# Optimization experiments

Hardware: AMD Instinct MI355X
Metric: run time of the kernel (lower is better)

The kernel has to match this reference:

```python
import jax, jax.numpy as jnp
import numpy as np

B = 256
H, W = 8, 16          # input_resolution for channels=256
C = 768               # dim = channels*3
WS = 4                # window_size
SHIFT = 2             # shift_size
NH = 12               # num_heads
HD = C // NH          # head_dim = 64
HID = 1024            # mlp hidden = channels*4
N = WS * WS           # tokens per window = 16
NW = (H // WS) * (W // WS)  # windows per image = 8
LN_EPS = 1e-5


def _rel_pos_index():
    coords = np.stack(np.meshgrid(np.arange(WS), np.arange(WS), indexing='ij'))  # [2,ws,ws]
    cf = coords.reshape(2, -1)                      # [2, N]
    rel = (cf[:, :, None] - cf[:, None, :]).transpose(1, 2, 0)  # [N, N, 2]
    rel[:, :, 0] += WS - 1
    rel[:, :, 1] += WS - 1
    rel[:, :, 0] *= 2 * WS - 1
    return jnp.asarray(rel.sum(-1))                 # [N, N] int


def _attn_mask():
    img = np.zeros((H, W))
    slices = (slice(0, -WS), slice(-WS, -SHIFT), slice(-SHIFT, None))
    cnt = 0
    for hs in slices:
        for ws_ in slices:
            img[hs, ws_] = cnt
            cnt += 1
    mw = img.reshape(H // WS, WS, W // WS, WS).transpose(0, 2, 1, 3).reshape(-1, N)  # [nW, N]
    am = mw[:, None, :] - mw[:, :, None]            # [nW, N, N]
    return jnp.asarray(np.where(am != 0, -100.0, 0.0).astype(np.float32))


REL_IDX = _rel_pos_index()
ATTN_MASK = _attn_mask()


def _ln(x, g, b):
    m = x.mean(-1, keepdims=True)
    v = ((x - m) ** 2).mean(-1, keepdims=True)
    return (x - m) / jnp.sqrt(v + LN_EPS) * g + b


def setup_inputs() -> dict:
    key = jax.random.key(0)
    ks = jax.random.split(key, 8)
    s = 0.02
    return {
        'x': jax.random.normal(ks[0], (B, H * W, C), jnp.float32),
        'ln1_g': jnp.ones((C,), jnp.float32),
        'ln1_b': jnp.zeros((C,), jnp.float32),
        'qkv_w': jax.random.normal(ks[1], (C, 3 * C), jnp.float32) * s,
        'qkv_b': jnp.zeros((3 * C,), jnp.float32),
        'proj_w': jax.random.normal(ks[2], (C, C), jnp.float32) * s,
        'proj_b': jnp.zeros((C,), jnp.float32),
        'rel_table': jax.random.normal(ks[3], ((2 * WS - 1) * (2 * WS - 1), NH), jnp.float32) * s,
        'ln2_g': jnp.ones((C,), jnp.float32),
        'ln2_b': jnp.zeros((C,), jnp.float32),
        'fc1_w': jax.random.normal(ks[4], (C, HID), jnp.float32) * s,
        'fc1_b': jax.random.normal(ks[5], (HID,), jnp.float32) * 1e-6,
        'fc2_w': jax.random.normal(ks[6], (HID, C), jnp.float32) * s,
        'fc2_b': jax.random.normal(ks[7], (C,), jnp.float32) * 1e-6,
    }


def reference(x, ln1_g, ln1_b, qkv_w, qkv_b, proj_w, proj_b, rel_table,
              ln2_g, ln2_b, fc1_w, fc1_b, fc2_w, fc2_b):
    # --- norm1 + cyclic shift + window partition ---
    h = _ln(x, ln1_g, ln1_b).reshape(B, H, W, C)
    h = jnp.roll(h, (-SHIFT, -SHIFT), axis=(1, 2))
    hw = h.reshape(B, H // WS, WS, W // WS, WS, C).transpose(0, 1, 3, 2, 4, 5)
    hw = hw.reshape(B * NW, N, C)                   # (num_windows*B, N, C)
    # --- window attention with relative position bias + shift mask ---
    qkv = (hw @ qkv_w + qkv_b).reshape(B * NW, N, 3, NH, HD).transpose(2, 0, 3, 1, 4)
    q, k, v = qkv[0] * (HD ** -0.5), qkv[1], qkv[2]  # [Bn, NH, N, HD]
    attn = jnp.einsum('bhnd,bhmd->bhnm', q, k)      # [Bn, NH, N, N]
    bias = rel_table[REL_IDX].transpose(2, 0, 1)    # [NH, N, N]
    attn = attn + bias[None]
    attn = attn.reshape(B, NW, NH, N, N) + ATTN_MASK[None, :, None]
    attn = jax.nn.softmax(attn.reshape(B * NW, NH, N, N), axis=-1)
    o = jnp.einsum('bhnm,bhmd->bhnd', attn, v).transpose(0, 2, 1, 3).reshape(B * NW, N, C)
    o = o @ proj_w + proj_b
    # --- window reverse + reverse shift + residual ---
    o = o.reshape(B, H // WS, W // WS, WS, WS, C).transpose(0, 1, 3, 2, 4, 5).reshape(B, H, W, C)
    o = jnp.roll(o, (SHIFT, SHIFT), axis=(1, 2)).reshape(B, H * W, C)
    x = x + o
    # --- MLP block (dropout is identity at inference) ---
    y = _ln(x, ln2_g, ln2_b)
    y = jax.nn.gelu(y @ fc1_w + fc1_b, approximate=False)
    return x + (y @ fc2_w + fc2_b)
```

## Files before the change

kernel.cpp:

```cpp
#include <hip/hip_runtime.h>
#include <stdint.h>
#include <stddef.h>

typedef __attribute__((ext_vector_type(8))) short bf16x8;
typedef __attribute__((ext_vector_type(4))) float f32x4;
typedef __attribute__((ext_vector_type(4))) unsigned int uint4v;

static __device__ __forceinline__ unsigned short f2bf(float f) {
  unsigned int u = __builtin_bit_cast(unsigned int, f);
  unsigned int r = (u + 0x7FFFu + ((u >> 16) & 1u)) >> 16;
  return (unsigned short)r;
}
static __device__ __forceinline__ float bf2f(unsigned short h) {
  unsigned int u = ((unsigned int)h) << 16;
  return __builtin_bit_cast(float, u);
}

static __device__ __forceinline__ void gld16(const void* g, void* l) {
  __builtin_amdgcn_global_load_lds(
      (const __attribute__((address_space(1))) void*)g,
      (__attribute__((address_space(3))) void*)l, 16, 0, 0);
}

__global__ void transpose_cast(const float* __restrict__ src,
                               unsigned short* __restrict__ dst, int R, int C) {
  __shared__ float tile[32][33];
  int c0 = blockIdx.x * 32, r0 = blockIdx.y * 32;
  int tx = threadIdx.x, ty = threadIdx.y;
  #pragma unroll
  for (int i = 0; i < 32; i += 8)
    tile[ty + i][tx] = src[(size_t)(r0 + ty + i) * C + c0 + tx];
  __syncthreads();
  #pragma unroll
  for (int i = 0; i < 32; i += 8)
    dst[(size_t)(c0 + ty + i) * R + r0 + tx] = f2bf(tile[tx][ty + i]);
}

static __device__ __forceinline__ float blksum256(float v, float* sb) {
  #pragma unroll
  for (int o = 32; o > 0; o >>= 1) v += __shfl_down(v, o, 64);
  int lane = threadIdx.x & 63, w = threadIdx.x >> 6;
  __syncthreads();
  if (lane == 0) sb[w] = v;
  __syncthreads();
  return sb[0] + sb[1] + sb[2] + sb[3];
}

template <int MODE>
__global__ __launch_bounds__(256) void ln_kernel(const float* __restrict__ xf,
                                                 const unsigned short* __restrict__ xb,
                                                 const float* __restrict__ gg,
                                                 const float* __restrict__ bb,
                                                 unsigned short* __restrict__ out) {
  __shared__ float sb[4];
  const int d = blockIdx.x;
  size_t srow;
  if (MODE == 0) {
    int b = d >> 7, wid = (d >> 4) & 7, tok = d & 15;
    int oh = (((wid >> 2) << 2) + (tok >> 2) + 2) & 7;
    int ow = (((wid & 3) << 2) + (tok & 3) + 2) & 15;
    srow = (size_t)(b << 7) + oh * 16 + ow;
  } else {
    srow = d;
  }
  const int t = threadIdx.x;
  float v0, v1, v2;
  if (MODE == 0) {
    const float* xr_ = xf + srow * 768;
    v0 = xr_[t]; v1 = xr_[t + 256]; v2 = xr_[t + 512];
  } else {
    const unsigned short* xr_ = xb + srow * 768;
    v0 = bf2f(xr_[t]); v1 = bf2f(xr_[t + 256]); v2 = bf2f(xr_[t + 512]);
  }
  float mean = blksum256(v0 + v1 + v2, sb) * (1.0f / 768.0f);
  float d0 = v0 - mean, d1 = v1 - mean, d2 = v2 - mean;
  float var = blksum256(d0 * d0 + d1 * d1 + d2 * d2, sb) * (1.0f / 768.0f);
  float rstd = rsqrtf(var + 1e-5f);
  size_t o = (size_t)d * 768;
  out[o + t]       = f2bf(d0 * rstd * gg[t] + bb[t]);
  out[o + t + 256] = f2bf(d1 * rstd * gg[t + 256] + bb[t + 256]);
  out[o + t + 512] = f2bf(d2 * rstd * gg[t + 512] + bb[t + 512]);
}

template <int EPI>
__global__ __launch_bounds__(512, 2) void gemm256(
    const unsigned short* __restrict__ A, const unsigned short* __restrict__ BT,
    const float* __restrict__ bias, float* __restrict__ outF,
    unsigned short* __restrict__ outB, const float* __restrict__ resid,
    const unsigned short* __restrict__ residB,
    int M, int N, int K, int NT) {
  __shared__ __align__(16) unsigned short sA[2][256 * 64];
  __shared__ __align__(16) unsigned short sB[2][256 * 64];

  const int tid = threadIdx.x;
  const int lane = tid & 63, wv = tid >> 6;
  const int wr = wv >> 2, wc = wv & 3;
  const int fr = lane & 15, q4 = (lane >> 4) << 2;

  const int nwg = gridDim.x;
  const int orig = blockIdx.x;
  const int swz = (orig & 7) * (nwg >> 3) + (orig >> 3);
  const int mt = swz / NT, nt = swz - mt * NT;
  const int m0 = mt << 8, n0 = nt << 8;

  const size_t K2 = (size_t)K * 2;

  const int srow = tid >> 3;
  const int sg = tid & 7;
  const int sgs = ((sg ^ (srow & 7)) << 4);
  const char* pA = (const char*)A + (size_t)(m0 + srow) * K2 + sgs;
  const char* pB = (const char*)BT + (size_t)(n0 + srow) * K2 + sgs;
  char* sdA = (char*)&sA[0][0] + (wv << 10);
  char* sdB = (char*)&sB[0][0] + (wv << 10);

  const int g0 = (((lane >> 4) ^ (fr & 7)) << 4);
  const int g1 = (((4 + (lane >> 4)) ^ (fr & 7)) << 4);
  const int arow = (wr << 7) + fr;
  const int brow = (wc << 6) + fr;

  f32x4 acc[8][4];
  #pragma unroll
  for (int i = 0; i < 8; ++i)
    #pragma unroll
    for (int j = 0; j < 4; ++j) acc[i][j] = (f32x4){0.f, 0.f, 0.f, 0.f};

  bf16x8 af[4][2];
  bf16x8 bbv[2][2][2];
  const int KT = K >> 6;
  const int NI = KT >> 1;

#define BARR __builtin_amdgcn_s_barrier()
#define LGKM0 asm volatile("s_waitcnt lgkmcnt(0)" ::: "memory")
#define VM6 asm volatile("s_waitcnt vmcnt(6)" ::: "memory")
#define VM0 asm volatile("s_waitcnt vmcnt(0)" ::: "memory")

#define LDA(CB, mh)                                                          \
  {                                                                          \
    const char* ba = ((const char*)&sA[0][0]) + (CB)*32768;                  \
    _Pragma("unroll") for (int fm = 0; fm < 4; ++fm) {                       \
      const int r = arow + (mh)*64 + fm * 16;                                \
      af[fm][0] = *(const bf16x8*)(ba + r * 128 + g0);                       \
      af[fm][1] = *(const bf16x8*)(ba + r * 128 + g1);                       \
    }                                                                        \
  }
#define LDB(CB, nh)                                                          \
  {                                                                          \
    const char* ba = ((const char*)&sB[0][0]) + (CB)*32768;                  \
    _Pragma("unroll") for (int fn = 0; fn < 2; ++fn) {                       \
      const int r = brow + (nh)*32 + fn * 16;                                \
      bbv[nh][fn][0] = *(const bf16x8*)(ba + r * 128 + g0);                  \
      bbv[nh][fn][1] = *(const bf16x8*)(ba + r * 128 + g1);                  \
    }                                                                        \
  }
#define STGA(CB, tt, j)                                                      \
  gld16(pA + (size_t)((j)*64) * K2 + ((size_t)(tt) << 7),                    \
        sdA + (CB)*32768 + (j)*8192);
#define STGB(CB, tt, j)                                                      \
  gld16(pB + (size_t)((j)*64) * K2 + ((size_t)(tt) << 7),                    \
        sdB + (CB)*32768 + (j)*8192);
#define MMAQ(mh, nh)                                                         \
  _Pragma("unroll") for (int fm = 0; fm < 4; ++fm)                           \
      _Pragma("unroll") for (int fn = 0; fn < 2; ++fn) {                     \
    f32x4* ac = &acc[(mh)*4 + fm][(nh)*2 + fn];                              \
    *ac = __builtin_amdgcn_mfma_f32_16x16x32_bf16(af[fm][0], bbv[nh][fn][0], \
                                                  *ac, 0, 0, 0);             \
    *ac = __builtin_amdgcn_mfma_f32_16x16x32_bf16(af[fm][1], bbv[nh][fn][1], \
                                                  *ac, 0, 0, 0);             \
  }
#define OPEN  BARR; LGKM0; __builtin_amdgcn_s_setprio(1)
#define CLOSE __builtin_amdgcn_s_setprio(0)

  #pragma unroll
  for (int j = 0; j < 4; ++j) { STGA(0, 0, j); STGB(0, 0, j); }
  STGA(1, 1, 0); STGA(1, 1, 2);
  STGB(1, 1, 0); STGB(1, 1, 1); STGB(1, 1, 2); STGB(1, 1, 3);
  VM6;
  BARR;

  for (int i = 0; i < NI; ++i) {
    const int s1 = 2 * i + 1, s2 = 2 * i + 2, s3 = 2 * i + 3;
    const bool gl = (i + 1 < NI);
    LDB(0, 0) LDA(0, 0)
    STGA(1, s1, 1); STGA(1, s1, 3);
    OPEN; MMAQ(0, 0); CLOSE; BARR;
    LDB(0, 1)
    if (gl) { STGA(0, s2, 0); STGA(0, s2, 2); }
    OPEN; MMAQ(0, 1); CLOSE; BARR;
    LDA(0, 1)
    if (gl) { STGB(0, s2, 0); STGB(0, s2, 1); }
    OPEN; MMAQ(1, 1); CLOSE; BARR;
    if (gl) { STGB(0, s2, 2); STGB(0, s2, 3); }
    OPEN; MMAQ(1, 0); CLOSE;
    if (gl) { VM6; } else { VM0; }
    BARR;
    LDB(1, 0) LDA(1, 0)
    if (gl) { STGA(0, s2, 1); STGA(0, s2, 3); }
    OPEN; MMAQ(0, 0); CLOSE; BARR;
    LDB(1, 1)
    if (gl) { STGA(1, s3, 0); STGA(1, s3, 2); }
    OPEN; MMAQ(0, 1); CLOSE; BARR;
    LDA(1, 1)
    if (gl) { STGB(1, s3, 0); STGB(1, s3, 1); }
    OPEN; MMAQ(1, 1); CLOSE; BARR;
    if (gl) { STGB(1, s3, 2); STGB(1, s3, 3); }
    OPEN; MMAQ(1, 0); CLOSE;
    if (gl) { VM6; }
    BARR;
  }
#undef BARR
#undef LGKM0
#undef VM6
#undef VM0
#undef LDA
#undef LDB
#undef STGA
#undef STGB
#undef MMAQ
#undef OPEN
#undef CLOSE

  #pragma unroll
  for (int ai = 0; ai < 8; ++ai) {
    #pragma unroll
    for (int bj = 0; bj < 4; ++bj) {
      const int col = n0 + (wc << 6) + bj * 16 + fr;
      const float bc = bias[col];
      #pragma unroll
      for (int i = 0; i < 4; ++i) {
        const int row = m0 + (wr << 7) + ai * 16 + q4 + i;
        float v = acc[ai][bj][i] + bc;
        if (EPI == 0) {
          outB[(size_t)row * N + col] = f2bf(v);
        } else if (EPI == 1) {
          int b = row >> 7, wid = (row >> 4) & 7, tok = row & 15;
          int oh = (((wid >> 2) << 2) + (tok >> 2) + 2) & 7;
          int ow = (((wid & 3) << 2) + (tok & 3) + 2) & 15;
          size_t di = ((size_t)(b << 7) + oh * 16 + ow) * 768 + col;
          outB[di] = f2bf(v + resid[di]);
        } else if (EPI == 2) {
          float g = 0.5f * v * (1.0f + erff(v * 0.70710678118f));
          outB[(size_t)row * N + col] = f2bf(g);
        } else {
          size_t di = (size_t)row * N + col;
          outF[di] = v + bf2f(residB[di]);
        }
      }
    }
  }
}

__global__ __launch_bounds__(64) void attn_win(const unsigned short* __restrict__ qkv,
                                               const float* __restrict__ rel_table,
                                               unsigned short* __restrict__ o) {
  __shared__ __align__(16) unsigned short q_s[16 * 64];
  __shared__ __align__(16) unsigned short k_s[16 * 64];
  __shared__ __align__(16) unsigned short vt_s[64 * 32];
  __shared__ __align__(16) unsigned short p_s[16 * 32];
  const int bid = blockIdx.x;
  const int win = bid / 12;
  const int head = bid - win * 12;
  const int wid = win & 7;
  const int lane = threadIdx.x;
  const unsigned short* gq =
      qkv + (size_t)win * 16 * 2304 + head * 64 + (size_t)(lane >> 2) * 2304 + ((lane & 3) << 4);
  const int t = lane >> 2, d0 = (lane & 3) << 4;
  *(uint4v*)&q_s[t * 64 + d0]     = *(const uint4v*)(gq);
  *(uint4v*)&q_s[t * 64 + d0 + 8] = *(const uint4v*)(gq + 8);
  *(uint4v*)&k_s[t * 64 + d0]     = *(const uint4v*)(gq + 768);
  *(uint4v*)&k_s[t * 64 + d0 + 8] = *(const uint4v*)(gq + 776);
  unsigned short vv[16];
  *(uint4v*)&vv[0] = *(const uint4v*)(gq + 1536);
  *(uint4v*)&vv[8] = *(const uint4v*)(gq + 1544);
  #pragma unroll
  for (int e = 0; e < 16; ++e) vt_s[(d0 + e) * 32 + t] = vv[e];
  #pragma unroll
  for (int e = 0; e < 16; ++e) vt_s[lane * 32 + 16 + e] = 0;
  if (lane < 16) {
    #pragma unroll
    for (int e = 0; e < 16; ++e) p_s[lane * 32 + 16 + e] = 0;
  }
  __syncthreads();

  const int fr = lane & 15, kg = (lane >> 4) << 3;
  bf16x8 qa0 = *(const bf16x8*)&q_s[fr * 64 + kg];
  bf16x8 qa1 = *(const bf16x8*)&q_s[fr * 64 + 32 + kg];
  bf16x8 ka0 = *(const bf16x8*)&k_s[fr * 64 + kg];
  bf16x8 ka1 = *(const bf16x8*)&k_s[fr * 64 + 32 + kg];
  f32x4 s = (f32x4){0.f, 0.f, 0.f, 0.f};
  s = __builtin_amdgcn_mfma_f32_16x16x32_bf16(qa0, ka0, s, 0, 0, 0);
  s = __builtin_amdgcn_mfma_f32_16x16x32_bf16(qa1, ka1, s, 0, 0, 0);

  const int wh = wid >> 2, wwc = wid & 3;
  const int rj = fr >> 2, cj = fr & 3;
  const int rowm = wh * 4 + rj, colm = wwc * 4 + cj;
  const int rgm = (rowm < 4 ? 0 : (rowm < 6 ? 1 : 2)) * 3 +
                  (colm < 12 ? 0 : (colm < 14 ? 1 : 2));
  float p[4];
  #pragma unroll
  for (int i = 0; i < 4; ++i) {
    int n = ((lane >> 4) << 2) + i;
    int ri = n >> 2, ci = n & 3;
    int rown = wh * 4 + ri, coln = wwc * 4 + ci;
    int rgn = (rown < 4 ? 0 : (rown < 6 ? 1 : 2)) * 3 +
              (coln < 12 ? 0 : (coln < 14 ? 1 : 2));
    float bias = rel_table[(size_t)((ri - rj + 3) * 7 + (ci - cj + 3)) * 12 + head];
    p[i] = s[i] * 0.125f + bias + (rgn != rgm ? -100.0f : 0.0f);
  }
  float mx[4] = {p[0], p[1], p[2], p[3]};
  #pragma unroll
  for (int off = 8; off > 0; off >>= 1)
    #pragma unroll
    for (int i = 0; i < 4; ++i) mx[i] = fmaxf(mx[i], __shfl_xor(mx[i], off, 64));
  float sm[4];
  #pragma unroll
  for (int i = 0; i < 4; ++i) { p[i] = __expf(p[i] - mx[i]); sm[i] = p[i]; }
  #pragma unroll
  for (int off = 8; off > 0; off >>= 1)
    #pragma unroll
    for (int i = 0; i < 4; ++i) sm[i] += __shfl_xor(sm[i], off, 64);
  #pragma unroll
  for (int i = 0; i < 4; ++i)
    p_s[(((lane >> 4) << 2) + i) * 32 + fr] = f2bf(p[i] / sm[i]);
  __syncthreads();

  bf16x8 pa = *(const bf16x8*)&p_s[fr * 32 + kg];
  const f32x4 oz = (f32x4){0.f, 0.f, 0.f, 0.f};
  #pragma unroll
  for (int c = 0; c < 4; ++c) {
    bf16x8 vb = *(const bf16x8*)&vt_s[(c * 16 + fr) * 32 + kg];
    f32x4 oa = __builtin_amdgcn_mfma_f32_16x16x32_bf16(pa, vb, oz, 0, 0, 0);
    #pragma unroll
    for (int i = 0; i < 4; ++i) {
      int n = ((lane >> 4) << 2) + i;
      o[((size_t)win * 16 + n) * 768 + head * 64 + c * 16 + fr] = f2bf(oa[i]);
    }
  }
}

extern "C" void kernel_launch(void* const* d_in, const int* in_sizes, int n_in,
                              void* d_out, int out_size, void* d_ws, size_t ws_size,
                              hipStream_t stream) {
  const float* x      = (const float*)d_in[0];
  const float* ln1_g  = (const float*)d_in[1];
  const float* ln1_b  = (const float*)d_in[2];
  const float* qkv_w  = (const float*)d_in[3];
  const float* qkv_b  = (const float*)d_in[4];
  const float* proj_w = (const float*)d_in[5];
  const float* proj_b = (const float*)d_in[6];
  const float* rel_t  = (const float*)d_in[7];
  const float* ln2_g  = (const float*)d_in[8];
  const float* ln2_b  = (const float*)d_in[9];
  const float* fc1_w  = (const float*)d_in[10];
  const float* fc1_b  = (const float*)d_in[11];
  const float* fc2_w  = (const float*)d_in[12];
  const float* fc2_b  = (const float*)d_in[13];
  float* out = (float*)d_out;

  char* ws = (char*)d_ws;
  unsigned short* wsA = (unsigned short*)(ws);
  unsigned short* qkvb = (unsigned short*)(ws + 50331648);
  unsigned short* xr16 = (unsigned short*)(ws + 50331648);
  unsigned short* h1 = (unsigned short*)(ws + 201326592);
  unsigned short* qkv_wT = (unsigned short*)(ws + 268435456);
  unsigned short* proj_wT = (unsigned short*)(ws + 271974400);
  unsigned short* fc1_wT = (unsigned short*)(ws + 273154048);
  unsigned short* fc2_wT = (unsigned short*)(ws + 274726912);

  dim3 tb(32, 8);
  transpose_cast<<<dim3(2304 / 32, 768 / 32), tb, 0, stream>>>(qkv_w, qkv_wT, 768, 2304);
  transpose_cast<<<dim3(768 / 32, 768 / 32), tb, 0, stream>>>(proj_w, proj_wT, 768, 768);
  transpose_cast<<<dim3(1024 / 32, 768 / 32), tb, 0, stream>>>(fc1_w, fc1_wT, 768, 1024);
  transpose_cast<<<dim3(768 / 32, 1024 / 32), tb, 0, stream>>>(fc2_w, fc2_wT, 1024, 768);

  ln_kernel<0><<<32768, 256, 0, stream>>>(x, nullptr, ln1_g, ln1_b, wsA);
  gemm256<0><<<dim3(128 * 9), 512, 0, stream>>>(wsA, qkv_wT, qkv_b, nullptr, qkvb,
                                                nullptr, nullptr,
                                                32768, 2304, 768, 9);
  attn_win<<<24576, 64, 0, stream>>>(qkvb, rel_t, wsA);
  gemm256<1><<<dim3(128 * 3), 512, 0, stream>>>(wsA, proj_wT, proj_b, nullptr, xr16,
                                                x, nullptr,
                                                32768, 768, 768, 3);
  ln_kernel<2><<<32768, 256, 0, stream>>>(nullptr, xr16, ln2_g, ln2_b, wsA);
  gemm256<2><<<dim3(128 * 4), 512, 0, stream>>>(wsA, fc1_wT, fc1_b, nullptr, h1,
                                                nullptr, nullptr,
                                                32768, 1024, 768, 4);
  gemm256<3><<<dim3(128 * 3), 512, 0, stream>>>(h1, fc2_wT, fc2_b, out, nullptr,
                                                nullptr, xr16,
                                                32768, 768, 1024, 3);
}
```

Before: 513.0 us.

## Merge weight transposes, vectorize LayerNorm, load attention Q/K directly to registers

```diff
diff --git a/kernel.cpp b/kernel.cpp
--- a/kernel.cpp
+++ b/kernel.cpp
@@ -22,11 +22,20 @@
       (__attribute__((address_space(3))) void*)l, 16, 0, 0);
 }
 
-__global__ void transpose_cast(const float* __restrict__ src,
-                               unsigned short* __restrict__ dst, int R, int C) {
+__global__ void transpose_cast_all(const float* __restrict__ s0, unsigned short* __restrict__ d0,
+                                   const float* __restrict__ s1, unsigned short* __restrict__ d1,
+                                   const float* __restrict__ s2, unsigned short* __restrict__ d2,
+                                   const float* __restrict__ s3, unsigned short* __restrict__ d3) {
   __shared__ float tile[32][33];
-  int c0 = blockIdx.x * 32, r0 = blockIdx.y * 32;
-  int tx = threadIdx.x, ty = threadIdx.y;
+  const int b = blockIdx.x;
+  const float* src; unsigned short* dst; int R, C, nbx, bi;
+  if (b < 1728)      { src = s0; dst = d0; R = 768;  C = 2304; nbx = 72; bi = b; }
+  else if (b < 2304) { src = s1; dst = d1; R = 768;  C = 768;  nbx = 24; bi = b - 1728; }
+  else if (b < 3072) { src = s2; dst = d2; R = 768;  C = 1024; nbx = 32; bi = b - 2304; }
+  else               { src = s3; dst = d3; R = 1024; C = 768;  nbx = 24; bi = b - 3072; }
+  const int bx = bi % nbx, by = bi / nbx;
+  const int c0 = bx * 32, r0 = by * 32;
+  const int tx = threadIdx.x, ty = threadIdx.y;
   #pragma unroll
   for (int i = 0; i < 32; i += 8)
     tile[ty + i][tx] = src[(size_t)(r0 + ty + i) * C + c0 + tx];
@@ -64,22 +73,37 @@
     srow = d;
   }
   const int t = threadIdx.x;
-  float v0, v1, v2;
+  const bool ex = t < 128;
+  float a0, a1, b0 = 0.f, b1 = 0.f;
   if (MODE == 0) {
-    const float* xr_ = xf + srow * 768;
-    v0 = xr_[t]; v1 = xr_[t + 256]; v2 = xr_[t + 512];
+    const float2* f2 = (const float2*)(xf + srow * 768);
+    float2 p = f2[t]; a0 = p.x; a1 = p.y;
+    if (ex) { float2 q = f2[256 + t]; b0 = q.x; b1 = q.y; }
   } else {
-    const unsigned short* xr_ = xb + srow * 768;
-    v0 = bf2f(xr_[t]); v1 = bf2f(xr_[t + 256]); v2 = bf2f(xr_[t + 512]);
-  }
-  float mean = blksum256(v0 + v1 + v2, sb) * (1.0f / 768.0f);
-  float d0 = v0 - mean, d1 = v1 - mean, d2 = v2 - mean;
-  float var = blksum256(d0 * d0 + d1 * d1 + d2 * d2, sb) * (1.0f / 768.0f);
+    const unsigned int* u = (const unsigned int*)(xb + srow * 768);
+    unsigned int p = u[t];
+    a0 = bf2f((unsigned short)p); a1 = bf2f((unsigned short)(p >> 16));
+    if (ex) {
+      unsigned int q = u[256 + t];
+      b0 = bf2f((unsigned short)q); b1 = bf2f((unsigned short)(q >> 16));
+    }
+  }
+  float mean = blksum256(a0 + a1 + b0 + b1, sb) * (1.0f / 768.0f);
+  float da0 = a0 - mean, da1 = a1 - mean, db0 = b0 - mean, db1 = b1 - mean;
+  float var = blksum256(da0 * da0 + da1 * da1 + (ex ? db0 * db0 + db1 * db1 : 0.f), sb) *
+              (1.0f / 768.0f);
   float rstd = rsqrtf(var + 1e-5f);
-  size_t o = (size_t)d * 768;
-  out[o + t]       = f2bf(d0 * rstd * gg[t] + bb[t]);
-  out[o + t + 256] = f2bf(d1 * rstd * gg[t + 256] + bb[t + 256]);
-  out[o + t + 512] = f2bf(d2 * rstd * gg[t + 512] + bb[t + 512]);
+  const float2* g2 = (const float2*)gg;
+  const float2* be2 = (const float2*)bb;
+  unsigned int* o32 = (unsigned int*)(out + (size_t)d * 768);
+  float2 g = g2[t], be = be2[t];
+  o32[t] = (unsigned int)f2bf(da0 * rstd * g.x + be.x) |
+           ((unsigned int)f2bf(da1 * rstd * g.y + be.y) << 16);
+  if (ex) {
+    float2 gq = g2[256 + t], bq = be2[256 + t];
+    o32[256 + t] = (unsigned int)f2bf(db0 * rstd * gq.x + bq.x) |
+                   ((unsigned int)f2bf(db1 * rstd * gq.y + bq.y) << 16);
+  }
 }
 
 template <int EPI>
@@ -252,8 +276,6 @@
 __global__ __launch_bounds__(64) void attn_win(const unsigned short* __restrict__ qkv,
                                                const float* __restrict__ rel_table,
                                                unsigned short* __restrict__ o) {
-  __shared__ __align__(16) unsigned short q_s[16 * 64];
-  __shared__ __align__(16) unsigned short k_s[16 * 64];
   __shared__ __align__(16) unsigned short vt_s[64 * 32];
   __shared__ __align__(16) unsigned short p_s[16 * 32];
   const int bid = blockIdx.x;
@@ -261,16 +283,11 @@
   const int head = bid - win * 12;
   const int wid = win & 7;
   const int lane = threadIdx.x;
-  const unsigned short* gq =
-      qkv + (size_t)win * 16 * 2304 + head * 64 + (size_t)(lane >> 2) * 2304 + ((lane & 3) << 4);
+  const unsigned short* qb = qkv + (size_t)win * 16 * 2304 + head * 64;
   const int t = lane >> 2, d0 = (lane & 3) << 4;
-  *(uint4v*)&q_s[t * 64 + d0]     = *(const uint4v*)(gq);
-  *(uint4v*)&q_s[t * 64 + d0 + 8] = *(const uint4v*)(gq + 8);
-  *(uint4v*)&k_s[t * 64 + d0]     = *(const uint4v*)(gq + 768);
-  *(uint4v*)&k_s[t * 64 + d0 + 8] = *(const uint4v*)(gq + 776);
   unsigned short vv[16];
-  *(uint4v*)&vv[0] = *(const uint4v*)(gq + 1536);
-  *(uint4v*)&vv[8] = *(const uint4v*)(gq + 1544);
+  *(uint4v*)&vv[0] = *(const uint4v*)(qb + 1536 + (size_t)t * 2304 + d0);
+  *(uint4v*)&vv[8] = *(const uint4v*)(qb + 1544 + (size_t)t * 2304 + d0);
   #pragma unroll
   for (int e = 0; e < 16; ++e) vt_s[(d0 + e) * 32 + t] = vv[e];
   #pragma unroll
@@ -281,11 +298,12 @@
   }
   __syncthreads();
 
-  const int fr = lane & 15, kg = (lane >> 4) << 3;
-  bf16x8 qa0 = *(const bf16x8*)&q_s[fr * 64 + kg];
-  bf16x8 qa1 = *(const bf16x8*)&q_s[fr * 64 + 32 + kg];
-  bf16x8 ka0 = *(const bf16x8*)&k_s[fr * 64 + kg];
-  bf16x8 ka1 = *(const bf16x8*)&k_s[fr * 64 + 32 + kg];
+  const int fr = lane & 15, g8 = (lane >> 4) << 3;
+  const unsigned short* qrow = qb + (size_t)fr * 2304;
+  bf16x8 qa0 = *(const bf16x8*)(qrow + g8);
+  bf16x8 qa1 = *(const bf16x8*)(qrow + 32 + g8);
+  bf16x8 ka0 = *(const bf16x8*)(qrow + 768 + g8);
+  bf16x8 ka1 = *(const bf16x8*)(qrow + 800 + g8);
   f32x4 s = (f32x4){0.f, 0.f, 0.f, 0.f};
   s = __builtin_amdgcn_mfma_f32_16x16x32_bf16(qa0, ka0, s, 0, 0, 0);
   s = __builtin_amdgcn_mfma_f32_16x16x32_bf16(qa1, ka1, s, 0, 0, 0);
@@ -323,11 +341,11 @@
     p_s[(((lane >> 4) << 2) + i) * 32 + fr] = f2bf(p[i] / sm[i]);
   __syncthreads();
 
-  bf16x8 pa = *(const bf16x8*)&p_s[fr * 32 + kg];
+  bf16x8 pa = *(const bf16x8*)&p_s[fr * 32 + g8];
   const f32x4 oz = (f32x4){0.f, 0.f, 0.f, 0.f};
   #pragma unroll
   for (int c = 0; c < 4; ++c) {
-    bf16x8 vb = *(const bf16x8*)&vt_s[(c * 16 + fr) * 32 + kg];
+    bf16x8 vb = *(const bf16x8*)&vt_s[(c * 16 + fr) * 32 + g8];
     f32x4 oa = __builtin_amdgcn_mfma_f32_16x16x32_bf16(pa, vb, oz, 0, 0, 0);
     #pragma unroll
     for (int i = 0; i < 4; ++i) {
@@ -366,11 +384,8 @@
   unsigned short* fc1_wT = (unsigned short*)(ws + 273154048);
   unsigned short* fc2_wT = (unsigned short*)(ws + 274726912);
 
-  dim3 tb(32, 8);
-  transpose_cast<<<dim3(2304 / 32, 768 / 32), tb, 0, stream>>>(qkv_w, qkv_wT, 768, 2304);
-  transpose_cast<<<dim3(768 / 32, 768 / 32), tb, 0, stream>>>(proj_w, proj_wT, 768, 768);
-  transpose_cast<<<dim3(1024 / 32, 768 / 32), tb, 0, stream>>>(fc1_w, fc1_wT, 768, 1024);
-  transpose_cast<<<dim3(768 / 32, 1024 / 32), tb, 0, stream>>>(fc2_w, fc2_wT, 1024, 768);
+  transpose_cast_all<<<3840, dim3(32, 8), 0, stream>>>(qkv_w, qkv_wT, proj_w, proj_wT,
+                                                       fc1_w, fc1_wT, fc2_w, fc2_wT);
 
   ln_kernel<0><<<32768, 256, 0, stream>>>(x, nullptr, ln1_g, ln1_b, wsA);
   gemm256<0><<<dim3(128 * 9), 512, 0, stream>>>(wsA, qkv_wT, qkv_b, nullptr, qkvb,
```

Result: no change. 514.1 us (+0.2%).
